# Kernel optimization log

Hardware: AMD Instinct MI355X
Metric: run time of the kernel (lower is better)

Reference implementation:

```python
import jax, jax.numpy as jnp
import numpy as np

N = 50000      # nodes (B-rep faces)
E = 800000     # directed edges (avg degree 16)
F_IN = 9       # 8 surface-type flags + is_feature
H1, H2, C = 512, 128, 2


def setup_inputs() -> dict:
    key = jax.random.key(0)
    ks = jax.random.split(key, 8)
    x = jax.random.normal(ks[0], (N, F_IN), dtype=jnp.float32)
    edge_index = jax.random.randint(ks[1], (2, E), 0, N, dtype=jnp.int64)
    W1 = jax.random.normal(ks[2], (F_IN, H1), dtype=jnp.float32) / np.sqrt(F_IN)
    b1 = jnp.zeros((H1,), dtype=jnp.float32)
    W2 = jax.random.normal(ks[3], (H1, H2), dtype=jnp.float32) / np.sqrt(H1)
    b2 = jnp.zeros((H2,), dtype=jnp.float32)
    W3 = jax.random.normal(ks[4], (H2, C), dtype=jnp.float32) / np.sqrt(H2)
    b3 = jnp.zeros((C,), dtype=jnp.float32)
    return {"x": x, "W1": W1, "b1": b1, "W2": W2, "b2": b2,
            "W3": W3, "b3": b3, "edge_index": edge_index}


def reference(x, W1, b1, W2, b2, W3, b3, edge_index):
    n = x.shape[0]
    self_idx = jnp.arange(n, dtype=edge_index.dtype)
    # GCN with self-loops and symmetric normalization (PyG gcn_norm)
    src = jnp.concatenate([edge_index[0], self_idx])  # [E+N]
    dst = jnp.concatenate([edge_index[1], self_idx])  # [E+N]
    deg = jax.ops.segment_sum(jnp.ones_like(src, dtype=x.dtype), dst, num_segments=n)
    dinv = jnp.where(deg > 0, jax.lax.rsqrt(jnp.maximum(deg, 1.0)), 0.0)
    norm = dinv[src] * dinv[dst]  # [E+N]

    def gcn(h, W, b):
        h = h @ W                                   # [N, out]
        msg = h[src] * norm[:, None]                # gather + scale
        return jax.ops.segment_sum(msg, dst, num_segments=n) + b  # scatter-add

    h = jax.nn.relu(gcn(x, W1, b1))
    h = jax.nn.relu(gcn(h, W2, b2))
    # F.dropout with training=False is identity (inference mode)
    h = gcn(h, W3, b3)
    return jax.nn.log_softmax(h, axis=1)
```

## Files before the change

### kernel.cpp

```cpp
#include <hip/hip_runtime.h>
#include <hip/hip_bf16.h>

typedef __attribute__((ext_vector_type(8))) short short8;
typedef __attribute__((ext_vector_type(4))) float float4v;
typedef unsigned int uint;

#define NBLK 192

static __device__ __forceinline__ float2 up_bf2(uint v) {
    float2 r;
    r.x = __uint_as_float(v << 16);
    r.y = __uint_as_float(v & 0xffff0000u);
    return r;
}
static __device__ __forceinline__ short f2bf_bits(float x) {
    union { __hip_bfloat16 h; short s; } u;
    u.h = __float2bfloat16(x);
    return u.s;
}


__global__ __launch_bounds__(256) void k_hist(const int* __restrict__ dst, int E, int chunk,
        int shift, int nbuck, int* __restrict__ histBlk) {
    __shared__ int h[256];
    h[threadIdx.x] = 0;
    __syncthreads();
    int blk = blockIdx.x;
    int e0 = blk * chunk, e1 = min(E, e0 + chunk);
    for (int e = e0 + threadIdx.x; e < e1; e += 256)
        atomicAdd(&h[dst[e] >> shift], 1);
    __syncthreads();
    if (threadIdx.x < nbuck) histBlk[threadIdx.x * NBLK + blk] = h[threadIdx.x];
}


__global__ __launch_bounds__(256) void k_btot(const int* __restrict__ histBlk,
                                              int* __restrict__ btot) {
    __shared__ int s[256];
    int b = blockIdx.x, t = threadIdx.x;
    s[t] = (t < NBLK) ? histBlk[b * NBLK + t] : 0;
    __syncthreads();
    for (int off = 128; off; off >>= 1) {
        if (t < off) s[t] += s[t + off];
        __syncthreads();
    }
    if (t == 0) btot[b] = s[0];
}


__global__ __launch_bounds__(256) void k_bscan(const int* __restrict__ histBlk,
        const int* __restrict__ btot, int nbuck,
        int* __restrict__ baseBlk, int* __restrict__ bucketBase) {
    __shared__ int s[256], sb[256];
    int b = blockIdx.x, t = threadIdx.x;
    int v = (t < NBLK) ? histBlk[b * NBLK + t] : 0;
    s[t] = v;
    sb[t] = (t < nbuck) ? btot[t] : 0;
    __syncthreads();
    for (int off = 1; off < 256; off <<= 1) {
        int u = (t >= off) ? s[t - off] : 0;
        int u2 = (t >= off) ? sb[t - off] : 0;
        __syncthreads();
        s[t] += u;
        sb[t] += u2;
        __syncthreads();
    }
    int base = (b > 0) ? sb[b - 1] : 0;
    if (t < NBLK) baseBlk[b * NBLK + t] = base + s[t] - v;
    if (t == 0) bucketBase[b] = base;
}


__global__ __launch_bounds__(256) void k_scatterbin(const int* __restrict__ src,
        const int* __restrict__ dst, int E, int chunk, int shift, int nbuck,
        const int* __restrict__ baseBlk, uint* __restrict__ binned) {
    __shared__ int cur[256];
    int blk = blockIdx.x;
    if (threadIdx.x < nbuck) cur[threadIdx.x] = baseBlk[threadIdx.x * NBLK + blk];
    __syncthreads();
    int e0 = blk * chunk, e1 = min(E, e0 + chunk);
    int mask = (1 << shift) - 1;
    for (int e = e0 + threadIdx.x; e < e1; e += 256) {
        int d = dst[e];
        int pos = atomicAdd(&cur[d >> shift], 1);
        binned[pos] = (uint)src[e] | ((uint)(d & mask) << 24);
    }
}


__global__ __launch_bounds__(256) void k_csrbuild(const uint* __restrict__ binned,
        const int* __restrict__ bucketBase, const float* __restrict__ x,
        int E, int shift, int n, int nbuck,
        int* __restrict__ row_ptr, float* __restrict__ dinv, float* __restrict__ xs,
        int* __restrict__ csr) {
    __shared__ int cnt[256], lcur[256];
    int b = blockIdx.x, t = threadIdx.x;
    cnt[t] = 0;
    __syncthreads();
    int lo = bucketBase[b];
    int hi = (b + 1 < nbuck) ? bucketBase[b + 1] : E;
    for (int e = lo + t; e < hi; e += 256)
        atomicAdd(&cnt[binned[e] >> 24], 1);
    __syncthreads();
    int c = cnt[t];
    lcur[t] = c;
    __syncthreads();
    for (int off = 1; off < 256; off <<= 1) {
        int u = (t >= off) ? lcur[t - off] : 0;
        __syncthreads();
        lcur[t] += u;
        __syncthreads();
    }
    int node0 = b << shift;
    int nodeEnd = min(n, (b + 1) << shift);
    int cntNodes = nodeEnd - node0;
    int myBase = lo + lcur[t] - c;
    if (t < cntNodes) {
        row_ptr[node0 + t] = myBase;
        dinv[node0 + t] = rsqrtf((float)(c + 1));
    }
    if (b == nbuck - 1 && t == 0) row_ptr[n] = E;
    for (int j = t; j < cntNodes * 9; j += 256) {
        int nl = j / 9, f = j - nl * 9;
        float dnl = rsqrtf((float)(cnt[nl] + 1));
        xs[(size_t)(node0 + nl) * 9 + f] = dnl * x[(size_t)(node0 + nl) * 9 + f];
    }
    __syncthreads();
    lcur[t] = myBase;
    __syncthreads();
    for (int e = lo + t; e < hi; e += 256) {
        uint p = binned[e];
        int pos = atomicAdd(&lcur[p >> 24], 1);
        csr[pos] = (int)(p & 0xFFFFFF);
    }
}


__global__ __launch_bounds__(256) void k_agg1w(const float* __restrict__ xs,
                       const float* __restrict__ dinv,
                       const int* __restrict__ row_ptr, const int* __restrict__ csr,
                       const float* __restrict__ W1,
                       __hip_bfloat16* __restrict__ aggx_bf,
                       __hip_bfloat16* __restrict__ W1frag, int n, int nagg) {
    int bid = blockIdx.x;
    if (bid >= nagg) {
        int t = (bid - nagg) * 256 + threadIdx.x;
        if (t < 32 * 64) {
            int ctile = t >> 6, lane = t & 63;
            int col = ctile * 16 + (lane & 15);
            int k0 = (lane >> 4) * 8;
            short8 o;
#pragma unroll
            for (int j = 0; j < 8; ++j) {
                int k = k0 + j;
                o[j] = f2bf_bits(k < 9 ? W1[k * 512 + col] : 0.f);
            }
            *reinterpret_cast<short8*>(W1frag + (size_t)t * 8) = o;
        }
        return;
    }
    int node = bid * 8 + (threadIdx.x >> 5);
    if (node >= n) return;
    int l = threadIdx.x & 31;
    int slot = l >> 4;
    int f = l & 15;
    bool act = f < 9;
    float acc = (act && slot == 0) ? xs[node * 9 + f] : 0.f;
    int e0 = row_ptr[node], e1 = row_ptr[node + 1];
    int e = e0;
    for (; e + 16 <= e1; e += 16) {
        int si[8];
        float xv[8];
#pragma unroll
        for (int j = 0; j < 8; ++j) si[j] = csr[e + 2 * j + slot];
#pragma unroll
        for (int j = 0; j < 8; ++j) xv[j] = act ? xs[si[j] * 9 + f] : 0.f;
#pragma unroll
        for (int j = 0; j < 8; ++j) acc += xv[j];
    }
    for (; e + 4 <= e1; e += 4) {
        int s0 = csr[e + slot], s1 = csr[e + 2 + slot];
        float x0 = act ? xs[s0 * 9 + f] : 0.f;
        float x1 = act ? xs[s1 * 9 + f] : 0.f;
        acc += x0 + x1;
    }
    for (; e + 2 <= e1; e += 2) {
        int s0 = csr[e + slot];
        acc += act ? xs[s0 * 9 + f] : 0.f;
    }
    if (e < e1 && slot == 0) {
        int s0 = csr[e];
        acc += act ? xs[s0 * 9 + f] : 0.f;
    }
    acc += __shfl_xor(acc, 16);
    if (slot == 0) {
        float v = act ? dinv[node] * acc : 0.f;
        __hip_bfloat16* op = aggx_bf + (size_t)node * 32;
        union { __hip_bfloat16 h; short s; } u;
        u.h = __float2bfloat16(v);
        reinterpret_cast<short*>(op)[f] = u.s;
        reinterpret_cast<short*>(op)[16 + f] = 0;
    }
}


__global__ __launch_bounds__(512, 2) void k_l12(const __hip_bfloat16* __restrict__ aggx_bf,
                       const __hip_bfloat16* __restrict__ W1frag, const float* __restrict__ b1,
                       const float* __restrict__ W2, const float* __restrict__ dinv,
                       __hip_bfloat16* __restrict__ t2, int n, int npair) {
    __shared__ short bsh[64 * 128 * 8];
    __shared__ short h1s[8][2][16][40];
    int t = threadIdx.x;

    for (int idx = t; idx < 64 * 128; idx += 512) {
        int kb = idx >> 7, c = idx & 127;
        const float* wp = W2 + (size_t)(kb * 8) * 128 + c;
        short8 o;
#pragma unroll
        for (int j = 0; j < 8; ++j) o[j] = f2bf_bits(wp[j * 128]);
        *reinterpret_cast<short8*>(bsh + (size_t)idx * 8) = o;
    }
    __syncthreads();

    int wid = t >> 6, lane = t & 63;
    int pair = blockIdx.x * 8 + wid;
    if (pair >= npair) return;
    int r = lane & 15, quad = lane >> 4;
    short (*hs0)[40] = h1s[wid][0];
    short (*hs1)[40] = h1s[wid][1];

    int m0 = pair << 5;
    short8 aagg0 = *reinterpret_cast<const short8*>(
        aggx_bf + (size_t)(m0 + r) * 32 + quad * 8);
    short8 aagg1 = *reinterpret_cast<const short8*>(
        aggx_bf + (size_t)(m0 + 16 + r) * 32 + quad * 8);

    float4v acc0[8], acc1[8];
#pragma unroll
    for (int cg = 0; cg < 8; ++cg) {
        acc0[cg] = (float4v){0, 0, 0, 0};
        acc1[cg] = (float4v){0, 0, 0, 0};
    }

    for (int kt = 0; kt < 16; ++kt) {
        short8 bf0 = *reinterpret_cast<const short8*>(
            W1frag + ((size_t)(2 * kt) * 64 + lane) * 8);
        short8 bf1 = *reinterpret_cast<const short8*>(
            W1frag + ((size_t)(2 * kt + 1) * 64 + lane) * 8);
        float4v c00 = __builtin_amdgcn_mfma_f32_16x16x32_bf16(
            aagg0, bf0, (float4v){0, 0, 0, 0}, 0, 0, 0);
        float4v c01 = __builtin_amdgcn_mfma_f32_16x16x32_bf16(
            aagg0, bf1, (float4v){0, 0, 0, 0}, 0, 0, 0);
        float4v c10 = __builtin_amdgcn_mfma_f32_16x16x32_bf16(
            aagg1, bf0, (float4v){0, 0, 0, 0}, 0, 0, 0);
        float4v c11 = __builtin_amdgcn_mfma_f32_16x16x32_bf16(
            aagg1, bf1, (float4v){0, 0, 0, 0}, 0, 0, 0);
        float bb0 = b1[kt * 32 + r];
        float bb1 = b1[kt * 32 + 16 + r];
#pragma unroll
        for (int i = 0; i < 4; ++i) {
            int row = quad * 4 + i;
            hs0[row][r]      = f2bf_bits(fmaxf(c00[i] + bb0, 0.f));
            hs0[row][16 + r] = f2bf_bits(fmaxf(c01[i] + bb1, 0.f));
            hs1[row][r]      = f2bf_bits(fmaxf(c10[i] + bb0, 0.f));
            hs1[row][16 + r] = f2bf_bits(fmaxf(c11[i] + bb1, 0.f));
        }
        short8 am0 = *reinterpret_cast<const short8*>(&hs0[r][quad * 8]);
        short8 am1 = *reinterpret_cast<const short8*>(&hs1[r][quad * 8]);
#pragma unroll
        for (int cg = 0; cg < 8; ++cg) {
            short8 b = *reinterpret_cast<const short8*>(
                bsh + (size_t)(((kt * 4 + quad) * 128) + cg * 16 + r) * 8);
            acc0[cg] = __builtin_amdgcn_mfma_f32_16x16x32_bf16(am0, b, acc0[cg], 0, 0, 0);
            acc1[cg] = __builtin_amdgcn_mfma_f32_16x16x32_bf16(am1, b, acc1[cg], 0, 0, 0);
        }
    }

#pragma unroll
    for (int i = 0; i < 4; ++i) {
        int node0 = m0 + quad * 4 + i;
        if (node0 < n) {
            float di = dinv[node0];
            __hip_bfloat16* op = t2 + (size_t)node0 * 128 + r;
#pragma unroll
            for (int cg = 0; cg < 8; ++cg)
                op[cg * 16] = __float2bfloat16(di * acc0[cg][i]);
        }
        int node1 = m0 + 16 + quad * 4 + i;
        if (node1 < n) {
            float di = dinv[node1];
            __hip_bfloat16* op = t2 + (size_t)node1 * 128 + r;
#pragma unroll
            for (int cg = 0; cg < 8; ++cg)
                op[cg * 16] = __float2bfloat16(di * acc1[cg][i]);
        }
    }
}


__global__ __launch_bounds__(256) void k_agg2(const uint* __restrict__ t2u,
                       const float* __restrict__ dinv,
                       const int* __restrict__ row_ptr, const int* __restrict__ csr,
                       const float* __restrict__ b2, const float* __restrict__ W3,
                       float2* __restrict__ t3, int n) {
    int node = blockIdx.x * 4 + (threadIdx.x >> 6);
    if (node >= n) return;
    int lane = threadIdx.x & 63;
    int half = lane >> 5;
    int cl = lane & 31;
    const uint2* t2v = reinterpret_cast<const uint2*>(t2u);

    float a0 = 0.f, a1 = 0.f, a2 = 0.f, a3 = 0.f;
    if (half == 0) {
        uint2 sv = t2v[(size_t)node * 32 + cl];
        float2 pa = up_bf2(sv.x), pb = up_bf2(sv.y);
        a0 = pa.x; a1 = pa.y; a2 = pb.x; a3 = pb.y;
    }

    int e0 = row_ptr[node], e1 = row_ptr[node + 1];
    int eb = e0;
    for (; eb + 16 <= e1; eb += 16) {
        int si[8];
        uint2 ri[8];
#pragma unroll
        for (int j = 0; j < 8; ++j) si[j] = csr[eb + half + 2 * j];
#pragma unroll
        for (int j = 0; j < 8; ++j) ri[j] = t2v[(size_t)si[j] * 32 + cl];
#pragma unroll
        for (int j = 0; j < 8; ++j) {
            float2 qa = up_bf2(ri[j].x), qb = up_bf2(ri[j].y);
            a0 += qa.x; a1 += qa.y; a2 += qb.x; a3 += qb.y;
        }
    }
    for (; eb + 4 <= e1; eb += 4) {
        int s0 = csr[eb + half], s1 = csr[eb + half + 2];
        uint2 r0 = t2v[(size_t)s0 * 32 + cl];
        uint2 r1 = t2v[(size_t)s1 * 32 + cl];
        float2 qa = up_bf2(r0.x), qb = up_bf2(r0.y);
        float2 qc = up_bf2(r1.x), qd = up_bf2(r1.y);
        a0 += qa.x + qc.x; a1 += qa.y + qc.y;
        a2 += qb.x + qd.x; a3 += qb.y + qd.y;
    }
    for (int e = eb + half; e < e1; e += 2) {
        uint2 rv = t2v[(size_t)csr[e] * 32 + cl];
        float2 qa = up_bf2(rv.x), qb = up_bf2(rv.y);
        a0 += qa.x; a1 += qa.y; a2 += qb.x; a3 += qb.y;
    }

    a0 += __shfl_xor(a0, 32);
    a1 += __shfl_xor(a1, 32);
    a2 += __shfl_xor(a2, 32);
    a3 += __shfl_xor(a3, 32);

    float di = dinv[node];
    float4 bb = *reinterpret_cast<const float4*>(b2 + 4 * cl);
    float h0 = fmaxf(di * a0 + bb.x, 0.f);
    float h1v = fmaxf(di * a1 + bb.y, 0.f);
    float h2 = fmaxf(di * a2 + bb.z, 0.f);
    float h3 = fmaxf(di * a3 + bb.w, 0.f);
    float4 wlo = *reinterpret_cast<const float4*>(W3 + 8 * cl);
    float4 whi = *reinterpret_cast<const float4*>(W3 + 8 * cl + 4);
    float c0 = h0 * wlo.x + h1v * wlo.z + h2 * whi.x + h3 * whi.z;
    float c1 = h0 * wlo.y + h1v * wlo.w + h2 * whi.y + h3 * whi.w;
#pragma unroll
    for (int off = 16; off; off >>= 1) {
        c0 += __shfl_xor(c0, off);
        c1 += __shfl_xor(c1, off);
    }
    if (lane == 0) t3[node] = make_float2(di * c0, di * c1);
}


__global__ void k_agg3(const float2* __restrict__ t3, const float* __restrict__ dinv,
                       const int* __restrict__ row_ptr, const int* __restrict__ csr,
                       const float* __restrict__ b3, float2* __restrict__ outv, int n) {
    int node = blockIdx.x * blockDim.x + threadIdx.x;
    if (node >= n) return;
    float2 s = t3[node];
    float a0 = s.x, a1 = s.y;
    int e0 = row_ptr[node], e1 = row_ptr[node + 1];
    int e = e0;
    for (; e + 4 <= e1; e += 4) {
        int s0 = csr[e], s1 = csr[e + 1], s2 = csr[e + 2], s3 = csr[e + 3];
        float2 q0 = t3[s0], q1 = t3[s1], q2 = t3[s2], q3 = t3[s3];
        a0 += q0.x + q1.x + q2.x + q3.x;
        a1 += q0.y + q1.y + q2.y + q3.y;
    }
    for (; e < e1; ++e) {
        float2 q0 = t3[csr[e]];
        a0 += q0.x;
        a1 += q0.y;
    }
    float di = dinv[node];
    float z0 = di * a0 + b3[0];
    float z1 = di * a1 + b3[1];
    float m = fmaxf(z0, z1);
    float lse = m + logf(expf(z0 - m) + expf(z1 - m));
    outv[node] = make_float2(z0 - lse, z1 - lse);
}


extern "C" void kernel_launch(void* const* d_in, const int* in_sizes, int n_in,
                              void* d_out, int out_size, void* d_ws, size_t ws_size,
                              hipStream_t stream) {
    const float* x  = (const float*)d_in[0];
    const float* W1 = (const float*)d_in[1];
    const float* b1 = (const float*)d_in[2];
    const float* W2 = (const float*)d_in[3];
    const float* b2 = (const float*)d_in[4];
    const float* W3 = (const float*)d_in[5];
    const float* b3 = (const float*)d_in[6];
    const int* edges = (const int*)d_in[7];

    int n = in_sizes[0] / 9;
    int E = in_sizes[7] / 2;
    const int* src = edges;
    const int* dst = edges + E;

    char* p = (char*)d_ws;
    auto alloc = [&](size_t bytes) {
        char* q = p;
        p += (bytes + 511) & ~(size_t)511;
        return q;
    };
    float* dinv       = (float*)alloc((size_t)n * 4);
    int*   row_ptr    = (int*)alloc((size_t)(n + 1) * 4);
    int*   csr        = (int*)alloc((size_t)E * 4);
    int*   histBlk    = (int*)alloc((size_t)256 * NBLK * 4);
    int*   baseBlk    = (int*)alloc((size_t)256 * NBLK * 4);
    int*   btot       = (int*)alloc(256 * 4);
    int*   bucketBase = (int*)alloc(256 * 4);
    uint*  binned     = (uint*)alloc((size_t)E * 4);
    float* xs         = (float*)alloc((size_t)n * 9 * 4);
    __hip_bfloat16* aggx_bf = (__hip_bfloat16*)alloc((size_t)(n + 64) * 32 * 2);
    __hip_bfloat16* W1frag  = (__hip_bfloat16*)alloc((size_t)32 * 64 * 8 * 2);
    __hip_bfloat16* t2 = (__hip_bfloat16*)alloc((size_t)n * 128 * 2);
    float2* t3 = (float2*)alloc((size_t)n * 8);

    const int B = 256;
    int shift = 8;
    int nbuck = ((n - 1) >> shift) + 1;
    int chunk = (E + NBLK - 1) / NBLK;

    k_hist<<<NBLK, B, 0, stream>>>(dst, E, chunk, shift, nbuck, histBlk);
    k_btot<<<nbuck, B, 0, stream>>>(histBlk, btot);
    k_bscan<<<nbuck, B, 0, stream>>>(histBlk, btot, nbuck, baseBlk, bucketBase);
    k_scatterbin<<<NBLK, B, 0, stream>>>(src, dst, E, chunk, shift, nbuck, baseBlk, binned);
    k_csrbuild<<<nbuck, B, 0, stream>>>(binned, bucketBase, x, E, shift, n, nbuck,
                                        row_ptr, dinv, xs, csr);

    int nagg = (n + 7) / 8;
    k_agg1w<<<nagg + 8, B, 0, stream>>>(xs, dinv, row_ptr, csr, W1,
                                        aggx_bf, W1frag, n, nagg);

    int ntile = (n + 15) / 16;
    int npair = (ntile + 1) / 2;
    k_l12<<<(npair + 7) / 8, 512, 0, stream>>>(aggx_bf, W1frag, b1, W2, dinv, t2, n, npair);
    k_agg2<<<(n + 3) / 4, 256, 0, stream>>>((const uint*)t2, dinv, row_ptr, csr, b2, W3, t3, n);

    k_agg3<<<(n + B - 1) / B, B, 0, stream>>>(t3, dinv, row_ptr, csr, b3, (float2*)d_out, n);
}
```

Before: 193.5 us.

## Fold bucket scan kernels into scatterbin and csrbuild prologues

Removes the separate k_btot and k_bscan launches. Each scatterbin and csrbuild block now recomputes bucket totals and exclusive prefix offsets from the per-block histogram. This saves two kernel launches and the baseBlk and bucketBase buffers. The cost is redundant work: every block has each thread serially read a 192-entry histogram row, which is strided, uncoalesced access.

```diff
diff --git a/kernel.cpp b/kernel.cpp
--- a/kernel.cpp
+++ b/kernel.cpp
@@ -34,53 +34,34 @@
 }
 
 
-__global__ __launch_bounds__(256) void k_btot(const int* __restrict__ histBlk,
-                                              int* __restrict__ btot) {
-    __shared__ int s[256];
-    int b = blockIdx.x, t = threadIdx.x;
-    s[t] = (t < NBLK) ? histBlk[b * NBLK + t] : 0;
-    __syncthreads();
-    for (int off = 128; off; off >>= 1) {
-        if (t < off) s[t] += s[t + off];
-        __syncthreads();
-    }
-    if (t == 0) btot[b] = s[0];
-}
-
-
-__global__ __launch_bounds__(256) void k_bscan(const int* __restrict__ histBlk,
-        const int* __restrict__ btot, int nbuck,
-        int* __restrict__ baseBlk, int* __restrict__ bucketBase) {
-    __shared__ int s[256], sb[256];
-    int b = blockIdx.x, t = threadIdx.x;
-    int v = (t < NBLK) ? histBlk[b * NBLK + t] : 0;
-    s[t] = v;
-    sb[t] = (t < nbuck) ? btot[t] : 0;
+__global__ __launch_bounds__(256) void k_scatterbin(const int* __restrict__ src,
+        const int* __restrict__ dst, int E, int chunk, int shift, int nbuck,
+        const int* __restrict__ histBlk, uint* __restrict__ binned) {
+    __shared__ int cur[256], s[256];
+    int blk = blockIdx.x, t = threadIdx.x;
+    int total = 0, partial = 0;
+    if (t < nbuck) {
+        const int* row = histBlk + t * NBLK;
+        for (int bl = 0; bl < NBLK; ++bl) {
+            int v = row[bl];
+            total += v;
+            if (bl < blk) partial += v;
+        }
+    }
+    s[t] = total;
     __syncthreads();
     for (int off = 1; off < 256; off <<= 1) {
         int u = (t >= off) ? s[t - off] : 0;
-        int u2 = (t >= off) ? sb[t - off] : 0;
         __syncthreads();
         s[t] += u;
-        sb[t] += u2;
-        __syncthreads();
-    }
-    int base = (b > 0) ? sb[b - 1] : 0;
-    if (t < NBLK) baseBlk[b * NBLK + t] = base + s[t] - v;
-    if (t == 0) bucketBase[b] = base;
-}
-
-
-__global__ __launch_bounds__(256) void k_scatterbin(const int* __restrict__ src,
-        const int* __restrict__ dst, int E, int chunk, int shift, int nbuck,
-        const int* __restrict__ baseBlk, uint* __restrict__ binned) {
-    __shared__ int cur[256];
-    int blk = blockIdx.x;
-    if (threadIdx.x < nbuck) cur[threadIdx.x] = baseBlk[threadIdx.x * NBLK + blk];
+        __syncthreads();
+    }
+    int base = (t > 0) ? s[t - 1] : 0;
+    if (t < nbuck) cur[t] = base + partial;
     __syncthreads();
     int e0 = blk * chunk, e1 = min(E, e0 + chunk);
     int mask = (1 << shift) - 1;
-    for (int e = e0 + threadIdx.x; e < e1; e += 256) {
+    for (int e = e0 + t; e < e1; e += 256) {
         int d = dst[e];
         int pos = atomicAdd(&cur[d >> shift], 1);
         binned[pos] = (uint)src[e] | ((uint)(d & mask) << 24);
@@ -89,16 +70,29 @@
 
 
 __global__ __launch_bounds__(256) void k_csrbuild(const uint* __restrict__ binned,
-        const int* __restrict__ bucketBase, const float* __restrict__ x,
+        const int* __restrict__ histBlk, const float* __restrict__ x,
         int E, int shift, int n, int nbuck,
         int* __restrict__ row_ptr, float* __restrict__ dinv, float* __restrict__ xs,
         int* __restrict__ csr) {
     __shared__ int cnt[256], lcur[256];
     int b = blockIdx.x, t = threadIdx.x;
     cnt[t] = 0;
-    __syncthreads();
-    int lo = bucketBase[b];
-    int hi = (b + 1 < nbuck) ? bucketBase[b + 1] : E;
+    int total = 0;
+    if (t < nbuck) {
+        const int* row = histBlk + t * NBLK;
+        for (int bl = 0; bl < NBLK; ++bl) total += row[bl];
+    }
+    lcur[t] = total;
+    __syncthreads();
+    for (int off = 1; off < 256; off <<= 1) {
+        int u = (t >= off) ? lcur[t - off] : 0;
+        __syncthreads();
+        lcur[t] += u;
+        __syncthreads();
+    }
+    int lo = (b > 0) ? lcur[b - 1] : 0;
+    int hi = lcur[b];
+    __syncthreads();
     for (int e = lo + t; e < hi; e += 256)
         atomicAdd(&cnt[binned[e] >> 24], 1);
     __syncthreads();
@@ -427,9 +421,6 @@
     int*   row_ptr    = (int*)alloc((size_t)(n + 1) * 4);
     int*   csr        = (int*)alloc((size_t)E * 4);
     int*   histBlk    = (int*)alloc((size_t)256 * NBLK * 4);
-    int*   baseBlk    = (int*)alloc((size_t)256 * NBLK * 4);
-    int*   btot       = (int*)alloc(256 * 4);
-    int*   bucketBase = (int*)alloc(256 * 4);
     uint*  binned     = (uint*)alloc((size_t)E * 4);
     float* xs         = (float*)alloc((size_t)n * 9 * 4);
     __hip_bfloat16* aggx_bf = (__hip_bfloat16*)alloc((size_t)(n + 64) * 32 * 2);
@@ -443,10 +434,8 @@
     int chunk = (E + NBLK - 1) / NBLK;
 
     k_hist<<<NBLK, B, 0, stream>>>(dst, E, chunk, shift, nbuck, histBlk);
-    k_btot<<<nbuck, B, 0, stream>>>(histBlk, btot);
-    k_bscan<<<nbuck, B, 0, stream>>>(histBlk, btot, nbuck, baseBlk, bucketBase);
-    k_scatterbin<<<NBLK, B, 0, stream>>>(src, dst, E, chunk, shift, nbuck, baseBlk, binned);
-    k_csrbuild<<<nbuck, B, 0, stream>>>(binned, bucketBase, x, E, shift, n, nbuck,
+    k_scatterbin<<<NBLK, B, 0, stream>>>(src, dst, E, chunk, shift, nbuck, histBlk, binned);
+    k_csrbuild<<<nbuck, B, 0, stream>>>(binned, histBlk, x, E, shift, n, nbuck,
                                         row_ptr, dinv, xs, csr);
 
     int nagg = (n + 7) / 8;
```

New measurement: 197.7 us. +2.2%, slower.
